# Kernel tuning notes

Measured on AMD Instinct MI355X. Metric: run time of the kernel, lower is better.

Reference implementation:

```python
import jax, jax.numpy as jnp
import numpy as np

EPS = 1e-20

def setup_inputs() -> dict:
    key = jax.random.key(0)
    k1, k2 = jax.random.split(key)
    x = jax.random.normal(k1, (8192, 4096), dtype=jnp.float32)
    weight = jax.random.normal(k2, (4096, 4096), dtype=jnp.float32)  # [out, in]
    return {"x": x, "weight": weight}

def reference(x, weight):
    # Binarize activations and weights with sign(v + eps), then matmul.
    xb = jnp.sign(x + EPS)
    wb = jnp.sign(weight + EPS)
    return jnp.matmul(xb, wb.T)  # [N, out]
```

## Files before the change

### kernel.cpp

```cpp
#include <hip/hip_runtime.h>
#include <stdint.h>

#define EPSF 1e-20f

typedef __attribute__((ext_vector_type(4))) int i32x4;
typedef __attribute__((ext_vector_type(8))) int i32x8;
typedef __attribute__((ext_vector_type(16))) float f32x16;


__global__ __launch_bounds__(256)
void bin_fp4_kernel(const float4* __restrict__ src, uint32_t* __restrict__ dst,
                    int n8) {
    int base = blockIdx.x * 1024 + threadIdx.x;
#pragma unroll
    for (int j = 0; j < 4; ++j) {
        int idx = base + j * 256;
        if (idx < n8) {
            float4 v0 = src[2 * idx];
            float4 v1 = src[2 * idx + 1];
            uint32_t w = 0;
            w |= ((v0.x < -EPSF) ? 0xAu : 0x2u);
            w |= ((v0.y < -EPSF) ? 0xAu : 0x2u) << 4;
            w |= ((v0.z < -EPSF) ? 0xAu : 0x2u) << 8;
            w |= ((v0.w < -EPSF) ? 0xAu : 0x2u) << 12;
            w |= ((v1.x < -EPSF) ? 0xAu : 0x2u) << 16;
            w |= ((v1.y < -EPSF) ? 0xAu : 0x2u) << 20;
            w |= ((v1.z < -EPSF) ? 0xAu : 0x2u) << 24;
            w |= ((v1.w < -EPSF) ? 0xAu : 0x2u) << 28;
            dst[idx] = w;
        }
    }
}

#define SCALE_ONE 0x7F7F7F7Fu

__global__ __launch_bounds__(512, 2)
void fp4mfma_gemm256(const char* __restrict__ x4, const char* __restrict__ w4,
                     float* __restrict__ out) {
    __shared__ char lds[2][65536];

    const int t = threadIdx.x;
    const int lane = t & 63;
    const int wave = t >> 6;
    const int wm = (wave >> 2) * 128;
    const int wn = (wave & 3) * 64;
    const int row0 = blockIdx.y * 256;
    const int col0 = blockIdx.x * 256;
    const int lrow = lane & 31;
    const int half = lane >> 5;

    const char* xbase = x4 + (size_t)row0 * 2048;
    const char* wbase = w4 + (size_t)col0 * 2048;

    const int srow = t >> 3;
    const int sqg  = (t & 7) ^ (srow & 7);
    const int gsrc = srow * 2048 + sqg * 16;
    const int gdst = t * 16;

    f32x16 acc[4][2];
#pragma unroll
    for (int r = 0; r < 4; ++r)
#pragma unroll
        for (int c = 0; c < 2; ++c)
#pragma unroll
            for (int e = 0; e < 16; ++e) acc[r][c][e] = 0.0f;

    i32x8 a8[2], b8[2];
#pragma unroll
    for (int r = 0; r < 2; ++r)
#pragma unroll
        for (int e = 0; e < 8; ++e) { a8[r][e] = 0; b8[r][e] = 0; }

    int qs16[4];
#pragma unroll
    for (int m = 0; m < 4; ++m)
        qs16[m] = (((2 * m + half) ^ (lrow & 7)) << 4);

    const int aoff = (wm + lrow) * 128;
    const int boff = (wn + lrow) * 128;

#define ISSUE_A(buf, g, kb)                                                   \
    __builtin_amdgcn_global_load_lds(                                         \
        (const uint32_t*)(xbase + (g) * 131072 + gsrc + (kb)),                \
        (uint32_t*)((buf) + (g) * 8192 + gdst), 16, 0, 0)
#define ISSUE_B(buf, g, kb)                                                   \
    __builtin_amdgcn_global_load_lds(                                         \
        (const uint32_t*)(wbase + (g) * 131072 + gsrc + (kb)),                \
        (uint32_t*)((buf) + 32768 + (g) * 8192 + gdst), 16, 0, 0)

    {
        char* b0 = &lds[0][0];
        ISSUE_A(b0, 0, 0); ISSUE_A(b0, 2, 0); ISSUE_B(b0, 0, 0); ISSUE_B(b0, 1, 0);
        ISSUE_B(b0, 2, 0); ISSUE_B(b0, 3, 0); ISSUE_A(b0, 1, 0); ISSUE_A(b0, 3, 0);
    }

    i32x4 bv[2][4];

    for (int kt = 0; kt < 16; ++kt) {
        char* cbuf = &lds[kt & 1][0];
        char* nbuf = &lds[(kt & 1) ^ 1][0];
        const int kb = (kt + 1) * 128;
        const bool st = (kt < 15);

        asm volatile("s_waitcnt vmcnt(2)" ::: "memory");
        __builtin_amdgcn_s_barrier();
        asm volatile("" ::: "memory");
        if (st) {
            ISSUE_A(nbuf, 0, kb); ISSUE_A(nbuf, 2, kb);
            ISSUE_B(nbuf, 0, kb); ISSUE_B(nbuf, 1, kb);
        }
#pragma unroll
        for (int m = 0; m < 4; ++m) {
#pragma unroll
            for (int r = 0; r < 2; ++r) {
                i32x4 av = *(const i32x4*)(cbuf + aoff + r * 4096 + qs16[m]);
                a8[r][0] = av[0]; a8[r][1] = av[1];
                a8[r][2] = av[2]; a8[r][3] = av[3];
            }
#pragma unroll
            for (int c = 0; c < 2; ++c) {
                bv[c][m] = *(const i32x4*)(cbuf + 32768 + boff + c * 4096 + qs16[m]);
                b8[c][0] = bv[c][m][0]; b8[c][1] = bv[c][m][1];
                b8[c][2] = bv[c][m][2]; b8[c][3] = bv[c][m][3];
            }
            __builtin_amdgcn_s_setprio(1);
#pragma unroll
            for (int r = 0; r < 2; ++r)
#pragma unroll
                for (int c = 0; c < 2; ++c)
                    acc[r][c] = __builtin_amdgcn_mfma_scale_f32_32x32x64_f8f6f4(
                        a8[r], b8[c], acc[r][c],
                        4, 4, 0, SCALE_ONE, 0, SCALE_ONE);
            __builtin_amdgcn_s_setprio(0);
        }

        if (st) { asm volatile("s_waitcnt vmcnt(4)" ::: "memory"); }
        else    { asm volatile("s_waitcnt vmcnt(0)" ::: "memory"); }
        __builtin_amdgcn_s_barrier();
        asm volatile("" ::: "memory");
        if (st) {
            ISSUE_B(nbuf, 2, kb); ISSUE_B(nbuf, 3, kb);
            ISSUE_A(nbuf, 1, kb); ISSUE_A(nbuf, 3, kb);
        }
#pragma unroll
        for (int m = 0; m < 4; ++m) {
#pragma unroll
            for (int r = 0; r < 2; ++r) {
                i32x4 av = *(const i32x4*)(cbuf + aoff + (2 + r) * 4096 + qs16[m]);
                a8[r][0] = av[0]; a8[r][1] = av[1];
                a8[r][2] = av[2]; a8[r][3] = av[3];
            }
#pragma unroll
            for (int c = 0; c < 2; ++c) {
                b8[c][0] = bv[c][m][0]; b8[c][1] = bv[c][m][1];
                b8[c][2] = bv[c][m][2]; b8[c][3] = bv[c][m][3];
            }
            __builtin_amdgcn_s_setprio(1);
#pragma unroll
            for (int r = 0; r < 2; ++r)
#pragma unroll
                for (int c = 0; c < 2; ++c)
                    acc[2 + r][c] = __builtin_amdgcn_mfma_scale_f32_32x32x64_f8f6f4(
                        a8[r], b8[c], acc[2 + r][c],
                        4, 4, 0, SCALE_ONE, 0, SCALE_ONE);
            __builtin_amdgcn_s_setprio(0);
        }
    }
#undef ISSUE_A
#undef ISSUE_B

#pragma unroll
    for (int r = 0; r < 4; ++r)
#pragma unroll
        for (int c = 0; c < 2; ++c)
#pragma unroll
            for (int e = 0; e < 16; ++e) {
                int rr = row0 + wm + r * 32 + (e & 3) + 8 * (e >> 2) + 4 * half;
                int cc = col0 + wn + c * 32 + lrow;
                out[(size_t)rr * 4096 + cc] = acc[r][c][e];
            }
}


__global__ __launch_bounds__(256)
void binarize_kernel(const float* __restrict__ src,
                     unsigned long long* __restrict__ dst, int n256) {
    int wave = blockIdx.x * 4 + (threadIdx.x >> 6);
    if (wave >= n256) return;
    int lane = threadIdx.x & 63;
    const float4* p = (const float4*)(src + (size_t)wave * 256);
    float4 v = p[lane];
    unsigned long long m0 = __ballot(v.x < -EPSF);
    unsigned long long m1 = __ballot(v.y < -EPSF);
    unsigned long long m2 = __ballot(v.z < -EPSF);
    unsigned long long m3 = __ballot(v.w < -EPSF);
    if (lane < 4) {
        unsigned long long m = (lane == 0) ? m0 : (lane == 1) ? m1
                             : (lane == 2) ? m2 : m3;
        dst[(size_t)wave * 4 + lane] = m;
    }
}

#define BM 128
#define BN 128
#define CHUNK_Q 8
#define NCHUNK 4
#define LDSS 9

__global__ __launch_bounds__(256, 2)
void bingemm_kernel(const uint4* __restrict__ xb, const uint4* __restrict__ wb,
                    float* __restrict__ out) {
    __shared__ uint4 xsl[BM * LDSS];
    __shared__ uint4 wsl[BN * LDSS];

    const int t  = threadIdx.x;
    const int tx = t & 15;
    const int ty = t >> 4;
    const int row0 = blockIdx.y * BM;
    const int col0 = blockIdx.x * BN;

    int acc[8][8];
#pragma unroll
    for (int a = 0; a < 8; ++a)
#pragma unroll
        for (int b = 0; b < 8; ++b) acc[a][b] = 0;

    const int srow = t >> 3;
    const int sq   = t & 7;

    for (int c = 0; c < NCHUNK; ++c) {
        __syncthreads();
#pragma unroll
        for (int k = 0; k < 4; ++k) {
            int r = srow + 32 * k;
            xsl[r * LDSS + sq] = xb[(size_t)(row0 + r) * 32 + c * CHUNK_Q + sq];
            wsl[r * LDSS + sq] = wb[(size_t)(col0 + r) * 32 + c * CHUNK_Q + sq];
        }
        __syncthreads();

#pragma unroll
        for (int q = 0; q < CHUNK_Q; ++q) {
            uint4 xq[8], wq[8];
#pragma unroll
            for (int ri = 0; ri < 8; ++ri)
                xq[ri] = xsl[(ty + 16 * ri) * LDSS + q];
#pragma unroll
            for (int cj = 0; cj < 8; ++cj)
                wq[cj] = wsl[(tx + 16 * cj) * LDSS + q];
#pragma unroll
            for (int ri = 0; ri < 8; ++ri)
#pragma unroll
                for (int cj = 0; cj < 8; ++cj) {
                    acc[ri][cj] += __builtin_popcount(xq[ri].x ^ wq[cj].x);
                    acc[ri][cj] += __builtin_popcount(xq[ri].y ^ wq[cj].y);
                    acc[ri][cj] += __builtin_popcount(xq[ri].z ^ wq[cj].z);
                    acc[ri][cj] += __builtin_popcount(xq[ri].w ^ wq[cj].w);
                }
        }
    }

#pragma unroll
    for (int ri = 0; ri < 8; ++ri) {
        size_t i = row0 + ty + 16 * ri;
#pragma unroll
        for (int cj = 0; cj < 8; ++cj) {
            int j = col0 + tx + 16 * cj;
            out[i * 4096 + j] = (float)(4096 - 2 * acc[ri][cj]);
        }
    }
}

extern "C" void kernel_launch(void* const* d_in, const int* in_sizes, int n_in,
                              void* d_out, int out_size, void* d_ws, size_t ws_size,
                              hipStream_t stream) {
    const float* x = (const float*)d_in[0];
    const float* w = (const float*)d_in[1];
    float* out = (float*)d_out;

    const int M = 8192, N = 4096, K = 4096;
    const size_t need_fp4 = ((size_t)M * K + (size_t)N * K) / 2;

    if (ws_size >= need_fp4) {
        char* x4 = (char*)d_ws;
        char* w4 = x4 + (size_t)M * K / 2;

        int n8x = (M * K) / 8;
        int n8w = (N * K) / 8;
        bin_fp4_kernel<<<n8x / 1024, 256, 0, stream>>>(
            (const float4*)x, (uint32_t*)x4, n8x);
        bin_fp4_kernel<<<n8w / 1024, 256, 0, stream>>>(
            (const float4*)w, (uint32_t*)w4, n8w);

        dim3 grid(N / 256, M / 256);
        fp4mfma_gemm256<<<grid, 512, 0, stream>>>(x4, w4, out);
    } else {
        uint32_t* xbits = (uint32_t*)d_ws;
        uint32_t* wbits = xbits + (size_t)M * (K / 32);

        binarize_kernel<<<(M * K) / 1024, 256, 0, stream>>>(
            x, (unsigned long long*)xbits, (M * K) / 256);
        binarize_kernel<<<(N * K) / 1024, 256, 0, stream>>>(
            w, (unsigned long long*)wbits, (N * K) / 256);

        dim3 grid(N / BN, M / BM);
        bingemm_kernel<<<grid, 256, 0, stream>>>(
            (const uint4*)xbits, (const uint4*)wbits, out);
    }
}
```

Before: 326.2 us.

## Restructure FP4 GEMM main loop into four ping-pong phases with staged LDS fragments

Splits each k-tile of the 256x256 FP4 MFMA GEMM into four phases. Each phase first loads A/B fragments from LDS into registers, then issues part of the next tile's global-to-LDS copies, then runs 8 MFMAs under raised priority, with explicit s_barrier and sched_barrier fences between phases. The goal is to interleave LDS reads, async global loads and MFMA work across the two resident workgroups in a ping-pong style, and to reuse B fragments across phases. The cost is extra barriers per k-tile and a tighter dependence on vmcnt accounting, where a wrong count could cause a race on the double-buffered LDS.

```diff
diff --git a/kernel.cpp b/kernel.cpp
--- a/kernel.cpp
+++ b/kernel.cpp
@@ -34,6 +34,10 @@
 
 #define SCALE_ONE 0x7F7F7F7Fu
 
+#define MFMA4(A8, B8, ACC)                                                  \
+    (ACC) = __builtin_amdgcn_mfma_scale_f32_32x32x64_f8f6f4(                \
+        (A8), (B8), (ACC), 4, 4, 0, SCALE_ONE, 0, SCALE_ONE)
+
 __global__ __launch_bounds__(512, 2)
 void fp4mfma_gemm256(const char* __restrict__ x4, const char* __restrict__ w4,
                      float* __restrict__ out) {
@@ -65,11 +69,13 @@
 #pragma unroll
             for (int e = 0; e < 16; ++e) acc[r][c][e] = 0.0f;
 
-    i32x8 a8[2], b8[2];
-#pragma unroll
-    for (int r = 0; r < 2; ++r)
-#pragma unroll
-        for (int e = 0; e < 8; ++e) { a8[r][e] = 0; b8[r][e] = 0; }
+    i32x8 a8[2], b8;
+#pragma unroll
+    for (int e = 0; e < 8; ++e) { a8[0][e] = 0; a8[1][e] = 0; b8[e] = 0; }
+
+    i32x4 aF[2][4];
+    i32x4 bF0[4];
+    i32x4 bF1[4];
 
     int qs16[4];
 #pragma unroll
@@ -77,7 +83,7 @@
         qs16[m] = (((2 * m + half) ^ (lrow & 7)) << 4);
 
     const int aoff = (wm + lrow) * 128;
-    const int boff = (wn + lrow) * 128;
+    const int boff = 32768 + (wn + lrow) * 128;
 
 #define ISSUE_A(buf, g, kb)                                                   \
     __builtin_amdgcn_global_load_lds(                                         \
@@ -90,81 +96,101 @@
 
     {
         char* b0 = &lds[0][0];
-        ISSUE_A(b0, 0, 0); ISSUE_A(b0, 2, 0); ISSUE_B(b0, 0, 0); ISSUE_B(b0, 1, 0);
-        ISSUE_B(b0, 2, 0); ISSUE_B(b0, 3, 0); ISSUE_A(b0, 1, 0); ISSUE_A(b0, 3, 0);
-    }
-
-    i32x4 bv[2][4];
+        ISSUE_B(b0, 0, 0); ISSUE_B(b0, 1, 0); ISSUE_B(b0, 2, 0); ISSUE_B(b0, 3, 0);
+        ISSUE_A(b0, 0, 0); ISSUE_A(b0, 2, 0); ISSUE_A(b0, 1, 0); ISSUE_A(b0, 3, 0);
+    }
+    asm volatile("s_waitcnt vmcnt(2)" ::: "memory");
+    __builtin_amdgcn_s_barrier();
 
     for (int kt = 0; kt < 16; ++kt) {
-        char* cbuf = &lds[kt & 1][0];
-        char* nbuf = &lds[(kt & 1) ^ 1][0];
+        const char* cb = &lds[kt & 1][0];
+        char* nb = &lds[(kt & 1) ^ 1][0];
         const int kb = (kt + 1) * 128;
         const bool st = (kt < 15);
 
-        asm volatile("s_waitcnt vmcnt(2)" ::: "memory");
-        __builtin_amdgcn_s_barrier();
-        asm volatile("" ::: "memory");
-        if (st) {
-            ISSUE_A(nbuf, 0, kb); ISSUE_A(nbuf, 2, kb);
-            ISSUE_B(nbuf, 0, kb); ISSUE_B(nbuf, 1, kb);
-        }
-#pragma unroll
-        for (int m = 0; m < 4; ++m) {
-#pragma unroll
-            for (int r = 0; r < 2; ++r) {
-                i32x4 av = *(const i32x4*)(cbuf + aoff + r * 4096 + qs16[m]);
-                a8[r][0] = av[0]; a8[r][1] = av[1];
-                a8[r][2] = av[2]; a8[r][3] = av[3];
-            }
-#pragma unroll
-            for (int c = 0; c < 2; ++c) {
-                bv[c][m] = *(const i32x4*)(cbuf + 32768 + boff + c * 4096 + qs16[m]);
-                b8[c][0] = bv[c][m][0]; b8[c][1] = bv[c][m][1];
-                b8[c][2] = bv[c][m][2]; b8[c][3] = bv[c][m][3];
-            }
-            __builtin_amdgcn_s_setprio(1);
-#pragma unroll
-            for (int r = 0; r < 2; ++r)
-#pragma unroll
-                for (int c = 0; c < 2; ++c)
-                    acc[r][c] = __builtin_amdgcn_mfma_scale_f32_32x32x64_f8f6f4(
-                        a8[r], b8[c], acc[r][c],
-                        4, 4, 0, SCALE_ONE, 0, SCALE_ONE);
-            __builtin_amdgcn_s_setprio(0);
-        }
-
+#pragma unroll
+        for (int m = 0; m < 4; ++m) {
+            aF[0][m] = *(const i32x4*)(cb + aoff + 0 * 4096 + qs16[m]);
+            aF[1][m] = *(const i32x4*)(cb + aoff + 1 * 4096 + qs16[m]);
+            bF0[m]   = *(const i32x4*)(cb + boff + 0 * 4096 + qs16[m]);
+        }
+        if (st) { ISSUE_B(nb, 0, kb); ISSUE_B(nb, 1, kb); }
+        __builtin_amdgcn_sched_barrier(0);
+        __builtin_amdgcn_s_barrier();
+        asm volatile("s_waitcnt lgkmcnt(0)" ::: "memory");
+        __builtin_amdgcn_sched_barrier(0);
+        __builtin_amdgcn_s_setprio(1);
+#pragma unroll
+        for (int m = 0; m < 4; ++m) {
+            *(i32x4*)&a8[0] = aF[0][m];
+            *(i32x4*)&a8[1] = aF[1][m];
+            *(i32x4*)&b8 = bF0[m];
+            MFMA4(a8[0], b8, acc[0][0]);
+            MFMA4(a8[1], b8, acc[1][0]);
+        }
+        __builtin_amdgcn_s_setprio(0);
+        __builtin_amdgcn_s_barrier();
+
+#pragma unroll
+        for (int m = 0; m < 4; ++m)
+            bF1[m] = *(const i32x4*)(cb + boff + 1 * 4096 + qs16[m]);
+        if (st) { ISSUE_B(nb, 2, kb); ISSUE_B(nb, 3, kb); }
+        __builtin_amdgcn_sched_barrier(0);
+        __builtin_amdgcn_s_barrier();
+        asm volatile("s_waitcnt lgkmcnt(0)" ::: "memory");
+        __builtin_amdgcn_sched_barrier(0);
+        __builtin_amdgcn_s_setprio(1);
+#pragma unroll
+        for (int m = 0; m < 4; ++m) {
+            *(i32x4*)&a8[0] = aF[0][m];
+            *(i32x4*)&a8[1] = aF[1][m];
+            *(i32x4*)&b8 = bF1[m];
+            MFMA4(a8[0], b8, acc[0][1]);
+            MFMA4(a8[1], b8, acc[1][1]);
+        }
+        __builtin_amdgcn_s_setprio(0);
         if (st) { asm volatile("s_waitcnt vmcnt(4)" ::: "memory"); }
         else    { asm volatile("s_waitcnt vmcnt(0)" ::: "memory"); }
         __builtin_amdgcn_s_barrier();
-        asm volatile("" ::: "memory");
-        if (st) {
-            ISSUE_B(nbuf, 2, kb); ISSUE_B(nbuf, 3, kb);
-            ISSUE_A(nbuf, 1, kb); ISSUE_A(nbuf, 3, kb);
-        }
-#pragma unroll
-        for (int m = 0; m < 4; ++m) {
-#pragma unroll
-            for (int r = 0; r < 2; ++r) {
-                i32x4 av = *(const i32x4*)(cbuf + aoff + (2 + r) * 4096 + qs16[m]);
-                a8[r][0] = av[0]; a8[r][1] = av[1];
-                a8[r][2] = av[2]; a8[r][3] = av[3];
-            }
-#pragma unroll
-            for (int c = 0; c < 2; ++c) {
-                b8[c][0] = bv[c][m][0]; b8[c][1] = bv[c][m][1];
-                b8[c][2] = bv[c][m][2]; b8[c][3] = bv[c][m][3];
-            }
-            __builtin_amdgcn_s_setprio(1);
-#pragma unroll
-            for (int r = 0; r < 2; ++r)
-#pragma unroll
-                for (int c = 0; c < 2; ++c)
-                    acc[2 + r][c] = __builtin_amdgcn_mfma_scale_f32_32x32x64_f8f6f4(
-                        a8[r], b8[c], acc[2 + r][c],
-                        4, 4, 0, SCALE_ONE, 0, SCALE_ONE);
-            __builtin_amdgcn_s_setprio(0);
-        }
+
+#pragma unroll
+        for (int m = 0; m < 4; ++m) {
+            aF[0][m] = *(const i32x4*)(cb + aoff + 2 * 4096 + qs16[m]);
+            aF[1][m] = *(const i32x4*)(cb + aoff + 3 * 4096 + qs16[m]);
+        }
+        if (st) { ISSUE_A(nb, 0, kb); ISSUE_A(nb, 2, kb); }
+        __builtin_amdgcn_sched_barrier(0);
+        __builtin_amdgcn_s_barrier();
+        asm volatile("s_waitcnt lgkmcnt(0)" ::: "memory");
+        __builtin_amdgcn_sched_barrier(0);
+        __builtin_amdgcn_s_setprio(1);
+#pragma unroll
+        for (int m = 0; m < 4; ++m) {
+            *(i32x4*)&a8[0] = aF[0][m];
+            *(i32x4*)&a8[1] = aF[1][m];
+            *(i32x4*)&b8 = bF0[m];
+            MFMA4(a8[0], b8, acc[2][0]);
+            MFMA4(a8[1], b8, acc[3][0]);
+        }
+        __builtin_amdgcn_s_setprio(0);
+        __builtin_amdgcn_s_barrier();
+
+        if (st) { ISSUE_A(nb, 1, kb); ISSUE_A(nb, 3, kb); }
+        __builtin_amdgcn_sched_barrier(0);
+        __builtin_amdgcn_s_barrier();
+        __builtin_amdgcn_sched_barrier(0);
+        __builtin_amdgcn_s_setprio(1);
+#pragma unroll
+        for (int m = 0; m < 4; ++m) {
+            *(i32x4*)&a8[0] = aF[0][m];
+            *(i32x4*)&a8[1] = aF[1][m];
+            *(i32x4*)&b8 = bF1[m];
+            MFMA4(a8[0], b8, acc[2][1]);
+            MFMA4(a8[1], b8, acc[3][1]);
+        }
+        __builtin_amdgcn_s_setprio(0);
+        if (st) { asm volatile("s_waitcnt vmcnt(2)" ::: "memory"); }
+        __builtin_amdgcn_s_barrier();
     }
 #undef ISSUE_A
 #undef ISSUE_B
```

Result: no change. 331.8 us (+1.7%).
